# Kernel optimization log

Hardware: AMD Instinct MI355X
Metric: run time of the kernel (lower is better)

Reference implementation:

```python
import jax, jax.numpy as jnp
import numpy as np

NUM_TOKENS = 32000
BATCH = 8192
K = 10  # 'ten-hot'

def setup_inputs() -> dict:
    key = jax.random.key(0)
    x = jax.random.randint(key, (BATCH, K), 0, NUM_TOKENS, dtype=jnp.int64)
    return {"x": x}

def reference(x) -> jnp.ndarray:
    # Multi-hot encode: out[n, x[n, j]] = 1 for all j. Duplicate indices simply
    # re-write 1 (set, not add), matching the torch assignment semantics.
    B = x.shape[0]
    out = jnp.zeros((B, NUM_TOKENS), dtype=jnp.float32)
    rows = jnp.arange(B, dtype=x.dtype)[:, None]  # [B,1] broadcasts over K
    out = out.at[rows, x].set(1.0, mode="drop")
    return out
```

## Files before the change

### kernel.cpp

```cpp
#include <hip/hip_runtime.h>


#define NUM_TOKENS 32000
#define KHOT 10
#define BLOCK 256
#define FILL_GRID 256
#define TOTAL_F4 65536000
#define FILL_ITERS (TOTAL_F4 / (FILL_GRID * BLOCK))

typedef float f32x4 __attribute__((ext_vector_type(4)));

__global__ __launch_bounds__(BLOCK) void tenhot_fill0(f32x4* __restrict__ out) {
    size_t i = (size_t)blockIdx.x * BLOCK + threadIdx.x;
    const f32x4 z = {0.f, 0.f, 0.f, 0.f};
    #pragma unroll 1
    for (int k = 0; k < FILL_ITERS; ++k) {
        out[i] = z;
        i += (size_t)FILL_GRID * BLOCK;
    }
}

__global__ __launch_bounds__(BLOCK) void tenhot_scatter(
    const int* __restrict__ x, float* __restrict__ out, int total) {
    const int t = blockIdx.x * BLOCK + threadIdx.x;
    if (t < total) {
        const int idx = x[t];
        const int row = t / KHOT;
        if (idx >= 0 && idx < NUM_TOKENS) {
            out[(size_t)row * NUM_TOKENS + idx] = 1.0f;
        }
    }
}

extern "C" void kernel_launch(void* const* d_in, const int* in_sizes, int n_in,
                              void* d_out, int out_size, void* d_ws, size_t ws_size,
                              hipStream_t stream) {
    const int* x = (const int*)d_in[0];
    float* out = (float*)d_out;
    const int total = in_sizes[0];
    tenhot_fill0<<<FILL_GRID, BLOCK, 0, stream>>>((f32x4*)out);
    tenhot_scatter<<<(total + BLOCK - 1) / BLOCK, BLOCK, 0, stream>>>(x, out, total);
}
```

Baseline: 189.5 us.

## Fuse zero-fill and scatter into one kernel with per-block ownership filtering

Merges the zero-fill and scatter kernels into a single launch. Each block scans the whole index array, keeps in shared memory the hot positions that fall in the float4 slots it will zero, zeroes its strided slice, then writes the ones after a block barrier. This removes the second launch and the ordering dependency between kernels. In exchange every block reads all 81920 indices, which is redundant work. Entries past the MAXHOT shared-memory buffer would be silently dropped.

```diff
diff --git a/kernel.cpp b/kernel.cpp
--- a/kernel.cpp
+++ b/kernel.cpp
@@ -3,32 +3,57 @@
 
 #define NUM_TOKENS 32000
 #define KHOT 10
+#define F4_PER_ROW 8000
 #define BLOCK 256
-#define FILL_GRID 256
+#define GRID 256
+#define STRIDE (GRID * BLOCK)
 #define TOTAL_F4 65536000
-#define FILL_ITERS (TOTAL_F4 / (FILL_GRID * BLOCK))
+#define ITERS (TOTAL_F4 / STRIDE)
+#define MAXHOT 12288
 
 typedef float f32x4 __attribute__((ext_vector_type(4)));
+typedef int   i32x4 __attribute__((ext_vector_type(4)));
 
-__global__ __launch_bounds__(BLOCK) void tenhot_fill0(f32x4* __restrict__ out) {
-    size_t i = (size_t)blockIdx.x * BLOCK + threadIdx.x;
+__global__ __launch_bounds__(BLOCK) void TenHotEncodeLayer_53566832115799_kernel(
+    const int* __restrict__ x, float* __restrict__ out, int total) {
+    __shared__ unsigned hot[MAXHOT];
+    __shared__ int nHot;
+    if (threadIdx.x == 0) nHot = 0;
+    __syncthreads();
+
+    const unsigned b = blockIdx.x;
+
+    const i32x4* __restrict__ x4 = (const i32x4*)x;
+    const int n4 = total >> 2;
+    for (int v = threadIdx.x; v < n4; v += BLOCK) {
+        const i32x4 q = x4[v];
+        #pragma unroll
+        for (int u = 0; u < 4; ++u) {
+            const int e = 4 * v + u;
+            const int idx = q[u];
+            if (idx < 0 || idx >= NUM_TOKENS) continue;
+            const unsigned row = (unsigned)e / KHOT;
+            const unsigned g = row * F4_PER_ROW + ((unsigned)idx >> 2);
+            if (((g & (STRIDE - 1)) >> 8) != b) continue;
+            const int s = atomicAdd(&nHot, 1);
+            if (s < MAXHOT) hot[s] = row * (unsigned)NUM_TOKENS + (unsigned)idx;
+        }
+    }
+
+    f32x4* __restrict__ out4 = (f32x4*)out;
+    size_t i = (size_t)b * BLOCK + threadIdx.x;
     const f32x4 z = {0.f, 0.f, 0.f, 0.f};
     #pragma unroll 1
-    for (int k = 0; k < FILL_ITERS; ++k) {
-        out[i] = z;
-        i += (size_t)FILL_GRID * BLOCK;
+    for (int k = 0; k < ITERS; ++k) {
+        out4[i] = z;
+        i += (size_t)STRIDE;
     }
-}
 
-__global__ __launch_bounds__(BLOCK) void tenhot_scatter(
-    const int* __restrict__ x, float* __restrict__ out, int total) {
-    const int t = blockIdx.x * BLOCK + threadIdx.x;
-    if (t < total) {
-        const int idx = x[t];
-        const int row = t / KHOT;
-        if (idx >= 0 && idx < NUM_TOKENS) {
-            out[(size_t)row * NUM_TOKENS + idx] = 1.0f;
-        }
+    __syncthreads();
+
+    const int n = (nHot < MAXHOT) ? nHot : MAXHOT;
+    for (int o = threadIdx.x; o < n; o += BLOCK) {
+        out[hot[o]] = 1.0f;
     }
 }
 
@@ -38,6 +63,5 @@
     const int* x = (const int*)d_in[0];
     float* out = (float*)d_out;
     const int total = in_sizes[0];
-    tenhot_fill0<<<FILL_GRID, BLOCK, 0, stream>>>((f32x4*)out);
-    tenhot_scatter<<<(total + BLOCK - 1) / BLOCK, BLOCK, 0, stream>>>(x, out, total);
+    TenHotEncodeLayer_53566832115799_kernel<<<GRID, BLOCK, 0, stream>>>(x, out, total);
 }
```

Result: slower. 261.0 us (+37.7%).

## Bucket hot indices per fill thread and write output in one sweep

Applied to the files above, without the earlier changes.

Adds a bucketing pass that uses atomics to assign each hot index to the fill thread that owns its float4, storing a packed iteration number and lane mask. A sweep kernel sorts each thread's small list in LDS and writes every float4 once, with ones already set. This drops the separate scatter pass and its partial-line rewrites of memory that was just zeroed. In exchange it adds a memset, an atomic bucketing kernel and per-thread branching in the store loop, and it silently drops entries if more than 16 land in one bucket.

```diff
diff --git a/kernel.cpp b/kernel.cpp
--- a/kernel.cpp
+++ b/kernel.cpp
@@ -3,20 +3,84 @@
 
 #define NUM_TOKENS 32000
 #define KHOT 10
+#define F4_PER_ROW 8000
 #define BLOCK 256
-#define FILL_GRID 256
+#define GRID 256
+#define STRIDE (GRID * BLOCK)
 #define TOTAL_F4 65536000
-#define FILL_ITERS (TOTAL_F4 / (FILL_GRID * BLOCK))
+#define ITERS (TOTAL_F4 / STRIDE)
+#define NBUCKET STRIDE
+#define CAP 16
+#define WS_NEEDED (NBUCKET * 4 + NBUCKET * CAP * 2)
 
 typedef float f32x4 __attribute__((ext_vector_type(4)));
+
+__global__ __launch_bounds__(BLOCK) void tenhot_bucket(
+    const int* __restrict__ x, unsigned* __restrict__ cnt,
+    unsigned short* __restrict__ ent, int total) {
+    const int t = blockIdx.x * BLOCK + threadIdx.x;
+    if (t >= total) return;
+    const int idx = x[t];
+    if (idx < 0 || idx >= NUM_TOKENS) return;
+    const unsigned row = (unsigned)t / KHOT;
+    const unsigned g = row * F4_PER_ROW + ((unsigned)idx >> 2);
+    const unsigned w = g & (NBUCKET - 1);
+    const unsigned k = g >> 16;
+    const unsigned pos = atomicAdd(&cnt[w], 1u);
+    if (pos < CAP)
+        ent[w * CAP + pos] = (unsigned short)((k << 4) | (1u << (idx & 3)));
+}
+
+__global__ __launch_bounds__(BLOCK) void tenhot_sweep(
+    const unsigned* __restrict__ cnt, const unsigned short* __restrict__ ent,
+    f32x4* __restrict__ out4) {
+    __shared__ unsigned short lst[BLOCK][CAP];
+    const unsigned t = threadIdx.x;
+    const unsigned w = blockIdx.x * BLOCK + t;
+
+    unsigned n = cnt[w];
+    if (n > CAP) n = CAP;
+    for (unsigned s = 0; s < n; ++s) lst[t][s] = ent[w * CAP + s];
+    for (unsigned a = 1; a < n; ++a) {
+        const unsigned short e = lst[t][a];
+        int p = (int)a - 1;
+        while (p >= 0 && (unsigned)(lst[t][p] >> 4) > (unsigned)(e >> 4)) {
+            lst[t][p + 1] = lst[t][p];
+            --p;
+        }
+        lst[t][p + 1] = e;
+    }
+    unsigned cur = 0;
+    unsigned nextK = (cur < n) ? (unsigned)(lst[t][cur] >> 4) : 0xFFFFu;
+
+    size_t i = (size_t)blockIdx.x * BLOCK + t;
+    const f32x4 z = {0.f, 0.f, 0.f, 0.f};
+    #pragma unroll 1
+    for (unsigned k = 0; k < ITERS; ++k) {
+        f32x4 v = z;
+        if (k == nextK) {
+            do {
+                const unsigned m = lst[t][cur] & 0xFu;
+                if (m & 1u) v.x = 1.0f;
+                if (m & 2u) v.y = 1.0f;
+                if (m & 4u) v.z = 1.0f;
+                if (m & 8u) v.w = 1.0f;
+                ++cur;
+                nextK = (cur < n) ? (unsigned)(lst[t][cur] >> 4) : 0xFFFFu;
+            } while (nextK == k);
+        }
+        out4[i] = v;
+        i += (size_t)STRIDE;
+    }
+}
 
 __global__ __launch_bounds__(BLOCK) void tenhot_fill0(f32x4* __restrict__ out) {
     size_t i = (size_t)blockIdx.x * BLOCK + threadIdx.x;
     const f32x4 z = {0.f, 0.f, 0.f, 0.f};
     #pragma unroll 1
-    for (int k = 0; k < FILL_ITERS; ++k) {
+    for (int k = 0; k < ITERS; ++k) {
         out[i] = z;
-        i += (size_t)FILL_GRID * BLOCK;
+        i += (size_t)STRIDE;
     }
 }
 
@@ -26,9 +90,8 @@
     if (t < total) {
         const int idx = x[t];
         const int row = t / KHOT;
-        if (idx >= 0 && idx < NUM_TOKENS) {
+        if (idx >= 0 && idx < NUM_TOKENS)
             out[(size_t)row * NUM_TOKENS + idx] = 1.0f;
-        }
     }
 }
 
@@ -38,6 +101,14 @@
     const int* x = (const int*)d_in[0];
     float* out = (float*)d_out;
     const int total = in_sizes[0];
-    tenhot_fill0<<<FILL_GRID, BLOCK, 0, stream>>>((f32x4*)out);
-    tenhot_scatter<<<(total + BLOCK - 1) / BLOCK, BLOCK, 0, stream>>>(x, out, total);
+    if (ws_size >= (size_t)WS_NEEDED) {
+        unsigned* cnt = (unsigned*)d_ws;
+        unsigned short* ent = (unsigned short*)((char*)d_ws + NBUCKET * 4);
+        hipMemsetAsync(d_ws, 0, NBUCKET * 4, stream);
+        tenhot_bucket<<<(total + BLOCK - 1) / BLOCK, BLOCK, 0, stream>>>(x, cnt, ent, total);
+        tenhot_sweep<<<GRID, BLOCK, 0, stream>>>(cnt, ent, (f32x4*)out);
+    } else {
+        tenhot_fill0<<<GRID, BLOCK, 0, stream>>>((f32x4*)out);
+        tenhot_scatter<<<(total + BLOCK - 1) / BLOCK, BLOCK, 0, stream>>>(x, out, total);
+    }
 }
```

Result: slower. 204.6 us (+8.0%).
